# Performance work log

Hardware: AMD Instinct MI355X
Metric: run time of the kernel (lower is better)

Reference implementation:

```python
import jax, jax.numpy as jnp
import numpy as np

# Static dims (match init_kwargs / input_specs)
N, F, C, H, W = 1, 60, 31, 64, 64
DIM = 60          # embed dim == F
WS = 8            # window_size
NH = 6            # num_heads
HD = DIM // NH    # head dim = 10
SHIFT = WS // 2   # shift for odd blocks
NWIN_TOK = WS * WS
MLP_HID = 4 * DIM
EPS = 1e-5


def _rel_pos_index(ws):
    # standard Swin relative position index, computed once in numpy
    coords = np.stack(np.meshgrid(np.arange(ws), np.arange(ws), indexing='ij'))  # (2, ws, ws)
    coords = coords.reshape(2, -1)                                                # (2, ws*ws)
    rel = coords[:, :, None] - coords[:, None, :]                                 # (2, n, n)
    rel = rel.transpose(1, 2, 0)
    rel[..., 0] += ws - 1
    rel[..., 1] += ws - 1
    rel[..., 0] *= 2 * ws - 1
    return rel.sum(-1)                                                            # (n, n)

RPI = jnp.asarray(_rel_pos_index(WS))  # (64, 64) int


def _attn_mask(h, w, ws, shift):
    # mask for shifted-window attention: -100 where tokens come from different regions
    img = np.zeros((h, w))
    cnt = 0
    for hs in (slice(0, -ws), slice(-ws, -shift), slice(-shift, None)):
        for wsl in (slice(0, -ws), slice(-ws, -shift), slice(-shift, None)):
            img[hs, wsl] = cnt
            cnt += 1
    m = img.reshape(h // ws, ws, w // ws, ws).transpose(0, 2, 1, 3).reshape(-1, ws * ws)  # (nW, n)
    diff = m[:, None, :] - m[:, :, None]
    return jnp.asarray(np.where(diff != 0, -100.0, 0.0).astype(np.float32))               # (nW, n, n)

ATTN_MASK = _attn_mask(H, W, WS, SHIFT)


def _ln(x, g, b):
    mu = jnp.mean(x, axis=-1, keepdims=True)
    var = jnp.mean(jnp.square(x - mu), axis=-1, keepdims=True)
    return (x - mu) * jax.lax.rsqrt(var + EPS) * g + b


def _swin_block(x, shift, g1, b1, qkv_w, qkv_b, rpb, proj_w, proj_b,
                g2, b2, fc1_w, fc1_b, fc2_w, fc2_b):
    # x: (B, L=H*W, DIM)
    B = x.shape[0]
    shortcut = x
    h = _ln(x, g1, b1).reshape(B, H, W, DIM)
    if shift > 0:
        h = jnp.roll(h, (-shift, -shift), axis=(1, 2))
    # window partition -> (B*nW, n, DIM)
    win = h.reshape(B, H // WS, WS, W // WS, WS, DIM).transpose(0, 1, 3, 2, 4, 5)
    win = win.reshape(-1, NWIN_TOK, DIM)
    Bw = win.shape[0]
    # qkv projection (torch Linear: y = x @ W.T + b)
    qkv = win @ qkv_w.T + qkv_b                                   # (Bw, n, 3*DIM)
    qkv = qkv.reshape(Bw, NWIN_TOK, 3, NH, HD).transpose(2, 0, 3, 1, 4)
    q, k, v = qkv[0], qkv[1], qkv[2]                              # (Bw, NH, n, HD)
    scale = HD ** -0.5
    attn = jnp.einsum('bhnd,bhmd->bhnm', q * scale, k)            # (Bw, NH, n, n)
    bias = rpb[RPI.reshape(-1)].reshape(NWIN_TOK, NWIN_TOK, NH).transpose(2, 0, 1)
    attn = attn + bias[None]
    if shift > 0:
        nW = ATTN_MASK.shape[0]
        attn = attn.reshape(-1, nW, NH, NWIN_TOK, NWIN_TOK) + ATTN_MASK[None, :, None]
        attn = attn.reshape(-1, NH, NWIN_TOK, NWIN_TOK)
    attn = jax.nn.softmax(attn, axis=-1)
    out = jnp.einsum('bhnm,bhmd->bhnd', attn, v).transpose(0, 2, 1, 3).reshape(Bw, NWIN_TOK, DIM)
    out = out @ proj_w.T + proj_b
    # window reverse -> (B, H, W, DIM)
    out = out.reshape(B, H // WS, W // WS, WS, WS, DIM).transpose(0, 1, 3, 2, 4, 5)
    out = out.reshape(B, H, W, DIM)
    if shift > 0:
        out = jnp.roll(out, (shift, shift), axis=(1, 2))
    x = shortcut + out.reshape(B, H * W, DIM)
    # MLP with exact GELU (torch nn.GELU default)
    h2 = _ln(x, g2, b2)
    h2 = jax.nn.gelu(h2 @ fc1_w.T + fc1_b, approximate=False) @ fc2_w.T + fc2_b
    return x + h2


def setup_inputs() -> dict:
    key = jax.random.key(0)
    ks = jax.random.split(key, 16)
    s = 0.02
    inp = {
        'x': jax.random.normal(ks[0], (N, F, C, H, W), jnp.float32),
        'norm1_g': jnp.ones((2, DIM), jnp.float32),
        'norm1_b': jnp.zeros((2, DIM), jnp.float32),
        'qkv_w': jax.random.normal(ks[1], (2, 3 * DIM, DIM), jnp.float32) * s,
        'qkv_b': jnp.zeros((2, 3 * DIM), jnp.float32),
        'rpb': jax.random.normal(ks[2], (2, (2 * WS - 1) ** 2, NH), jnp.float32) * s,
        'proj_w': jax.random.normal(ks[3], (2, DIM, DIM), jnp.float32) * s,
        'proj_b': jnp.zeros((2, DIM), jnp.float32),
        'norm2_g': jnp.ones((2, DIM), jnp.float32),
        'norm2_b': jnp.zeros((2, DIM), jnp.float32),
        'fc1_w': jax.random.normal(ks[4], (2, MLP_HID, DIM), jnp.float32) * s,
        'fc1_b': jnp.zeros((2, MLP_HID), jnp.float32),
        'fc2_w': jax.random.normal(ks[5], (2, DIM, MLP_HID), jnp.float32) * s,
        'fc2_b': jnp.zeros((2, DIM), jnp.float32),
    }
    return inp


def reference(x, norm1_g, norm1_b, qkv_w, qkv_b, rpb, proj_w, proj_b,
              norm2_g, norm2_b, fc1_w, fc1_b, fc2_w, fc2_b):
    # (N, F, C, H, W) -> (N*C, F, H, W) -> patch embed (flatten) -> (B, L, DIM)
    out = jnp.transpose(x, (0, 2, 1, 3, 4)).reshape(N * C, F, H, W)
    out = out.reshape(N * C, F, H * W).transpose(0, 2, 1)  # (B, L, DIM)
    for i in range(2):
        shift = 0 if i % 2 == 0 else SHIFT
        out = _swin_block(out, shift,
                          norm1_g[i], norm1_b[i], qkv_w[i], qkv_b[i], rpb[i],
                          proj_w[i], proj_b[i], norm2_g[i], norm2_b[i],
                          fc1_w[i], fc1_b[i], fc2_w[i], fc2_b[i])
    # patch unembed -> (B, F, H, W) -> (N, C, F, H, W) -> transpose(1,2)
    out = out.transpose(0, 2, 1).reshape(N * C, F, H, W)
    out = out.reshape(N, C, F, H, W)
    return jnp.transpose(out, (0, 2, 1, 3, 4))
```

## Files before the change

kernel.cpp:

```cpp
#include <hip/hip_runtime.h>
#include <hip/hip_bf16.h>
#include <math.h>


#define NB 31
#define NTOK 4096
#define DIM 60
#define NTOT (NB*NTOK)
#define QK_SCALE 0.31622776601683794f

typedef __attribute__((ext_vector_type(8))) short bf16x8;
typedef __attribute__((ext_vector_type(4))) float f32x4;

__device__ __forceinline__ short f2b(float f){
    return __builtin_bit_cast(short, __float2bfloat16(f));
}
__device__ __forceinline__ float b2f(unsigned short u){
    union{unsigned u;float f;}v; v.u=((unsigned)u)<<16; return v.f;
}
__device__ __forceinline__ unsigned pk2(float a,float b){
    return (unsigned)(unsigned short)f2b(a) | ((unsigned)(unsigned short)f2b(b)<<16);
}
#define MFMA16(a,b,c) __builtin_amdgcn_mfma_f32_16x16x32_bf16(a,b,c,0,0,0)

#define PK_QKV  0
#define PK_PROJ 13824
#define PK_W1   18432
#define PK_W2   35712
#define PK_STRIDE 52608

__global__ __launch_bounds__(256) void pack_w(
    const float* __restrict__ qkv_w, const float* __restrict__ proj_w,
    const float* __restrict__ fc1_w, const float* __restrict__ fc2_w,
    const float* __restrict__ rpb, short* __restrict__ pk, float* __restrict__ btab)
{
    const int L = blockIdx.x;
    short* o = pk + (size_t)L * PK_STRIDE;
    const float* qw = qkv_w + L * 10800;
    const float* pw = proj_w + L * 3600;
    const float* w1 = fc1_w + L * 14400;
    const float* w2 = fc2_w + L * 14400;
    const float* rp = rpb + L * 1350;
    const int t0 = blockIdx.y * 256 + threadIdx.x;
    const int STP = 256 * 8;

    for (int i = t0; i < 192 * 72; i += STP) {
        int row = i / 72, k = i - row * 72;
        int p = row / 96, rg = row - p * 96;
        short v = 0;
        if (rg < 90 && k < 60) {
            int which = rg / 30, idx = rg - which * 30;
            int h = p * 3 + idx / 10, e = idx - (idx / 10) * 10;
            float wv = qw[(which * 60 + h * 10 + e) * 60 + k];
            if (which == 0) wv *= QK_SCALE;
            v = f2b(wv);
        }
        o[PK_QKV + i] = v;
    }
    for (int i = t0; i < 64 * 72; i += STP) {
        int n = i / 72, k = i - n * 72;
        o[PK_PROJ + i] = (n < 60 && k < 60) ? f2b(pw[n * 60 + k]) : (short)0;
    }
    for (int i = t0; i < 240 * 72; i += STP) {
        int n = i / 72, k = i - n * 72;
        o[PK_W1 + i] = (k < 60) ? f2b(w1[n * 60 + k]) : (short)0;
    }
    for (int i = t0; i < 64 * 264; i += STP) {
        int n = i / 264, k = i - n * 264;
        o[PK_W2 + i] = (n < 60 && k < 240) ? f2b(w2[n * 240 + k]) : (short)0;
    }
    float* bo = btab + (size_t)L * 4 * 24576;
    for (int i = t0; i < 4 * 24576; i += STP) {
        int c = i / 24576, rem = i - c * 24576;
        int h = rem >> 12, rem2 = rem & 4095;
        int ii = rem2 >> 6, j = rem2 & 63;
        int iy = ii >> 3, ix = ii & 7, jy = j >> 3, jx = j & 7;
        float v = rp[((iy - jy + 7) * 15 + (ix - jx + 7)) * 6 + h];
        int riy = (c & 2) ? (iy < 4 ? 1 : 2) : 0;
        int rix = (c & 1) ? (ix < 4 ? 1 : 2) : 0;
        int rjy = (c & 2) ? (jy < 4 ? 1 : 2) : 0;
        int rjx = (c & 1) ? (jx < 4 ? 1 : 2) : 0;
        if (riy != rjy || rix != rjx) v -= 100.f;
        bo[i] = v;
    }
}

template<int L>
__global__ __launch_bounds__(256, 5) void swin_layer(
    const void* __restrict__ xin_v, void* __restrict__ xout_v,
    const float* __restrict__ g1, const float* __restrict__ b1,
    const float* __restrict__ g2, const float* __restrict__ b2,
    const short* __restrict__ pk, const float* __restrict__ btab,
    const float* __restrict__ qkv_b, const float* __restrict__ proj_b,
    const float* __restrict__ fc1_b, const float* __restrict__ fc2_b)
{
    __shared__ __attribute__((aligned(16))) short R1[64 * 72];
    __shared__ __attribute__((aligned(16))) short R2[10112];

    const f32x4 Z4 = {0.f, 0.f, 0.f, 0.f};
    const bf16x8 Z8 = {0, 0, 0, 0, 0, 0, 0, 0};

    const int tid = threadIdx.x, blk = blockIdx.x;
    const int b = blk >> 6, w = blk & 63, wy = w >> 3, wx = w & 7;
    const int shift = L ? 4 : 0;
    const int cls = L ? (((wy == 7) ? 2 : 0) + ((wx == 7) ? 1 : 0)) : 0;

    const float* xf = (const float*)xin_v;
    const unsigned short* xb = (const unsigned short*)xin_v;

    for (int i = tid; i < 64 * 18; i += 256) {
        int row = i / 18, t = i - row * 18, bc = t / 3, k = t - bc * 3;
        *(int*)&R2[row * 104 + bc * 16 + 10 + 2 * k] = 0;
    }
    for (int i = tid; i < 3 * 216; i += 256) {
        int hl = i / 216, j = i - hl * 216;
        *(int*)&R2[6656 + (hl * 16 + 10) * 72 + 2 * j] = 0;
    }

    const int tk = tid >> 2, l4 = tid & 3;
    const int tok = (((wy * 8 + (tk >> 3) + shift) & 63) << 6)
                  + ((wx * 8 + (tk & 7) + shift) & 63);
    if (L == 0) {
        float xr[15]; float s = 0.f, s2 = 0.f;
#pragma unroll
        for (int dd = 0; dd < 15; ++dd) {
            float v = xf[(size_t)(l4 * 15 + dd) * NTOT + b * NTOK + tok];
            xr[dd] = v; s += v; s2 += v * v;
        }
        s  += __shfl_xor(s, 1);  s  += __shfl_xor(s, 2);
        s2 += __shfl_xor(s2, 1); s2 += __shfl_xor(s2, 2);
        const float mu = s * (1.f / 60.f);
        const float rs = rsqrtf(s2 * (1.f / 60.f) - mu * mu + 1e-5f);
#pragma unroll
        for (int dd = 0; dd < 15; ++dd) {
            int d = l4 * 15 + dd;
            R1[tk * 72 + d] = f2b((xr[dd] - mu) * rs * g1[d] + b1[d]);
        }
#pragma unroll
        for (int u = 0; u < 3; ++u) R1[tk * 72 + 60 + l4 * 3 + u] = 0;
    } else {
        float xr[16]; float s = 0.f, s2 = 0.f;
        const int nd = (l4 == 3) ? 6 : 8, c0 = l4 * 16;
        const unsigned* rp_ = (const unsigned*)(xb + ((size_t)b * NTOK + tok) * DIM) + l4 * 8;
#pragma unroll
        for (int j = 0; j < 8; ++j) {
            if (j < nd) {
                unsigned u = rp_[j];
                float v0 = b2f((unsigned short)(u & 0xffff));
                float v1 = b2f((unsigned short)(u >> 16));
                xr[2 * j] = v0; xr[2 * j + 1] = v1;
                s += v0 + v1; s2 += v0 * v0 + v1 * v1;
            }
        }
        s  += __shfl_xor(s, 1);  s  += __shfl_xor(s, 2);
        s2 += __shfl_xor(s2, 1); s2 += __shfl_xor(s2, 2);
        const float mu = s * (1.f / 60.f);
        const float rs = rsqrtf(s2 * (1.f / 60.f) - mu * mu + 1e-5f);
#pragma unroll
        for (int j = 0; j < 8; ++j) {
            if (j < nd) {
                int d = c0 + 2 * j;
                float n0 = (xr[2 * j] - mu) * rs * g1[d] + b1[d];
                float n1 = (xr[2 * j + 1] - mu) * rs * g1[d + 1] + b1[d + 1];
                *(unsigned*)&R1[tk * 72 + d] = pk2(n0, n1);
            }
        }
        if (l4 == 3) {
#pragma unroll
            for (int u = 0; u < 3; ++u) *(unsigned*)&R1[tk * 72 + 60 + 2 * u] = 0;
        }
    }

    const int lane = tid & 63, r16 = lane & 15, g = lane >> 4;
    const int m0 = (tid >> 6) << 4;

    int tok4[4];
#pragma unroll
    for (int r = 0; r < 4; ++r) {
        int row = m0 + g * 4 + r;
        tok4[r] = (((wy * 8 + (row >> 3) + shift) & 63) << 6)
                + ((wx * 8 + (row & 7) + shift) & 63);
    }

    bf16x8 a0 = *(const bf16x8*)&R1[(m0 + r16) * 72 + g * 8];
    bf16x8 a1 = *(const bf16x8*)&R1[(m0 + r16) * 72 + 32 + g * 8];
    const float* btc = btab + (size_t)cls * 24576 + (m0 + r16) * 64;

    for (int p = 0; p < 2; ++p) {
#pragma unroll
        for (int nt = 0; nt < 6; ++nt) {
            const short* wr = pk + PK_QKV + (size_t)(p * 96 + nt * 16 + r16) * 72;
            bf16x8 w0 = *(const bf16x8*)(wr + g * 8);
            bf16x8 w1v = *(const bf16x8*)(wr + 32 + g * 8);
            int c = nt * 16 + r16;
            int which = 0, hl = 0, e = 0; float bias = 0.f;
            if (c < 90) {
                which = c / 30; int idx = c - which * 30;
                hl = idx / 10; e = idx - hl * 10;
                bias = qkv_b[which * 60 + (p * 3 + hl) * 10 + e];
                if (which == 0) bias *= QK_SCALE;
            }
            f32x4 acc = {bias, bias, bias, bias};
            acc = MFMA16(a0, w0, acc);
            acc = MFMA16(a1, w1v, acc);
            if (c < 90) {
                if (which == 0) {
#pragma unroll
                    for (int r = 0; r < 4; ++r)
                        R2[(m0 + g * 4 + r) * 104 + hl * 16 + e] = f2b(acc[r]);
                } else if (which == 1) {
#pragma unroll
                    for (int r = 0; r < 4; ++r)
                        R2[(m0 + g * 4 + r) * 104 + 48 + hl * 16 + e] = f2b(acc[r]);
                } else {
#pragma unroll
                    for (int r = 0; r < 2; ++r)
                        *(unsigned*)&R2[6656 + (hl * 16 + e) * 72 + m0 + g * 4 + 2 * r] =
                            pk2(acc[2 * r], acc[2 * r + 1]);
                }
            }
        }
        __syncthreads();

        for (int hl = 0; hl < 3; ++hl) {
            const int h = p * 3 + hl;
            bf16x8 qa = Z8;
            if (g < 2) qa = *(const bf16x8*)&R2[(m0 + r16) * 104 + hl * 16 + g * 8];
            const float* bh = btc + h * 4096;
            f32x4 sv[4];
#pragma unroll
            for (int nt = 0; nt < 4; ++nt) {
                bf16x8 kb = Z8;
                if (g < 2) kb = *(const bf16x8*)&R2[(nt * 16 + r16) * 104 + 48 + hl * 16 + g * 8];
                sv[nt] = MFMA16(kb, qa, *(const f32x4*)&bh[nt * 16 + g * 4]);
            }
            float mx = -1e30f;
#pragma unroll
            for (int nt = 0; nt < 4; ++nt)
#pragma unroll
                for (int r = 0; r < 4; ++r) mx = fmaxf(mx, sv[nt][r]);
            mx = fmaxf(mx, __shfl_xor(mx, 16));
            mx = fmaxf(mx, __shfl_xor(mx, 32));
            float sum = 0.f;
#pragma unroll
            for (int nt = 0; nt < 4; ++nt)
#pragma unroll
                for (int r = 0; r < 4; ++r) {
                    float e = __expf(sv[nt][r] - mx);
                    sv[nt][r] = e; sum += e;
                }
            sum += __shfl_xor(sum, 16);
            sum += __shfl_xor(sum, 32);
            const float inv = 1.f / sum;

            unsigned qd00 = pk2(sv[0][0], sv[0][1]), qd01 = pk2(sv[0][2], sv[0][3]);
            unsigned qd10 = pk2(sv[1][0], sv[1][1]), qd11 = pk2(sv[1][2], sv[1][3]);
            unsigned qd20 = pk2(sv[2][0], sv[2][1]), qd21 = pk2(sv[2][2], sv[2][3]);
            unsigned qd30 = pk2(sv[3][0], sv[3][1]), qd31 = pk2(sv[3][2], sv[3][3]);
            const int sA = (r16 + ((g & 1) << 5)) << 2;
            const int sB = sA + 64;
            const bool hi = (g >> 1) & 1;
            union { unsigned u[4]; bf16x8 v; } pb0, pb1;
            {
                unsigned x0 = __builtin_amdgcn_ds_bpermute(sA, (int)qd00);
                unsigned y0 = __builtin_amdgcn_ds_bpermute(sA, (int)qd10);
                pb0.u[0] = hi ? y0 : x0;
                unsigned x1 = __builtin_amdgcn_ds_bpermute(sA, (int)qd01);
                unsigned y1 = __builtin_amdgcn_ds_bpermute(sA, (int)qd11);
                pb0.u[1] = hi ? y1 : x1;
                unsigned x2 = __builtin_amdgcn_ds_bpermute(sB, (int)qd00);
                unsigned y2 = __builtin_amdgcn_ds_bpermute(sB, (int)qd10);
                pb0.u[2] = hi ? y2 : x2;
                unsigned x3 = __builtin_amdgcn_ds_bpermute(sB, (int)qd01);
                unsigned y3 = __builtin_amdgcn_ds_bpermute(sB, (int)qd11);
                pb0.u[3] = hi ? y3 : x3;
                unsigned u0 = __builtin_amdgcn_ds_bpermute(sA, (int)qd20);
                unsigned v0 = __builtin_amdgcn_ds_bpermute(sA, (int)qd30);
                pb1.u[0] = hi ? v0 : u0;
                unsigned u1 = __builtin_amdgcn_ds_bpermute(sA, (int)qd21);
                unsigned v1 = __builtin_amdgcn_ds_bpermute(sA, (int)qd31);
                pb1.u[1] = hi ? v1 : u1;
                unsigned u2 = __builtin_amdgcn_ds_bpermute(sB, (int)qd20);
                unsigned v2 = __builtin_amdgcn_ds_bpermute(sB, (int)qd30);
                pb1.u[2] = hi ? v2 : u2;
                unsigned u3 = __builtin_amdgcn_ds_bpermute(sB, (int)qd21);
                unsigned v3 = __builtin_amdgcn_ds_bpermute(sB, (int)qd31);
                pb1.u[3] = hi ? v3 : u3;
            }
            bf16x8 va0 = *(const bf16x8*)&R2[6656 + (hl * 16 + r16) * 72 + g * 8];
            bf16x8 va1 = *(const bf16x8*)&R2[6656 + (hl * 16 + r16) * 72 + 32 + g * 8];
            f32x4 o = MFMA16(va0, pb0.v, Z4);
            o = MFMA16(va1, pb1.v, o);
            if (g < 2) {
                *(unsigned*)&R1[(m0 + r16) * 72 + h * 10 + g * 4]     = pk2(o[0] * inv, o[1] * inv);
                *(unsigned*)&R1[(m0 + r16) * 72 + h * 10 + g * 4 + 2] = pk2(o[2] * inv, o[3] * inv);
            } else if (g == 2) {
                *(unsigned*)&R1[(m0 + r16) * 72 + h * 10 + 8] = pk2(o[0] * inv, o[1] * inv);
            }
        }
        __syncthreads();
    }

    {
        bf16x8 oa0 = *(const bf16x8*)&R1[(m0 + r16) * 72 + g * 8];
        bf16x8 oa1 = *(const bf16x8*)&R1[(m0 + r16) * 72 + 32 + g * 8];
#pragma unroll
        for (int nt = 0; nt < 4; ++nt) {
            const short* wr = pk + PK_PROJ + (size_t)(nt * 16 + r16) * 72;
            bf16x8 w0 = *(const bf16x8*)(wr + g * 8);
            bf16x8 w1v = *(const bf16x8*)(wr + 32 + g * 8);
            int d = nt * 16 + r16;
            float pb_ = (d < 60) ? proj_b[d] : 0.f;
            f32x4 acc = {pb_, pb_, pb_, pb_};
            acc = MFMA16(oa0, w0, acc);
            acc = MFMA16(oa1, w1v, acc);
            if (d < 60) {
#pragma unroll
                for (int r = 0; r < 4; ++r) {
                    float res;
                    if (L == 0) res = xf[(size_t)d * NTOT + b * NTOK + tok4[r]];
                    else        res = b2f(xb[((size_t)b * NTOK + tok4[r]) * DIM + d]);
                    R1[(m0 + g * 4 + r) * 72 + d] = f2b(res + acc[r]);
                }
            }
        }
    }

    {
        float yr[15]; float s = 0.f, s2 = 0.f;
#pragma unroll
        for (int dd = 0; dd < 15; ++dd) {
            float v = b2f((unsigned short)R1[tk * 72 + dd * 4 + l4]);
            yr[dd] = v; s += v; s2 += v * v;
        }
        s  += __shfl_xor(s, 1);  s  += __shfl_xor(s, 2);
        s2 += __shfl_xor(s2, 1); s2 += __shfl_xor(s2, 2);
        const float mu = s * (1.f / 60.f);
        const float rs = rsqrtf(s2 * (1.f / 60.f) - mu * mu + 1e-5f);
#pragma unroll
        for (int dd = 0; dd < 15; ++dd) {
            int d = dd * 4 + l4;
            R2[tk * 136 + d] = f2b((yr[dd] - mu) * rs * g2[d] + b2[d]);
        }
#pragma unroll
        for (int u = 0; u < 3; ++u) R2[tk * 136 + 60 + l4 * 3 + u] = 0;
    }

    bf16x8 la0 = *(const bf16x8*)&R2[(m0 + r16) * 136 + g * 8];
    bf16x8 la1 = *(const bf16x8*)&R2[(m0 + r16) * 136 + 32 + g * 8];

    f32x4 acc2[4];
#pragma unroll
    for (int nt = 0; nt < 4; ++nt) {
        int d = nt * 16 + r16;
        float fb = (d < 60) ? fc2_b[d] : 0.f;
        acc2[nt] = (f32x4){fb, fb, fb, fb};
    }

#pragma unroll
    for (int nt = 0; nt < 8; ++nt) {
        const short* wr = pk + PK_W1 + (size_t)(nt * 16 + r16) * 72;
        bf16x8 w0 = *(const bf16x8*)(wr + g * 8);
        bf16x8 w1v = *(const bf16x8*)(wr + 32 + g * 8);
        int c = nt * 16 + r16;
        float fb = fc1_b[c];
        f32x4 acc = {fb, fb, fb, fb};
        acc = MFMA16(la0, w0, acc);
        acc = MFMA16(la1, w1v, acc);
#pragma unroll
        for (int r = 0; r < 4; ++r) {
            float u = acc[r];
            float zz = 1.5957691216057308f * u + 0.07135481178528657f * (u * u * u);
            float ge = u * __builtin_amdgcn_rcpf(1.f + __expf(-zz));
            R2[(m0 + g * 4 + r) * 136 + c] = f2b(ge);
        }
    }
#pragma unroll
    for (int kk = 0; kk < 4; ++kk) {
        bf16x8 ha = *(const bf16x8*)&R2[(m0 + r16) * 136 + kk * 32 + g * 8];
#pragma unroll
        for (int nt = 0; nt < 4; ++nt) {
            const short* wr = pk + PK_W2 + (size_t)(nt * 16 + r16) * 264 + kk * 32 + g * 8;
            acc2[nt] = MFMA16(ha, *(const bf16x8*)wr, acc2[nt]);
        }
    }
    *(int*)&R2[(m0 + r16) * 136 + 112 + g * 4]     = 0;
    *(int*)&R2[(m0 + r16) * 136 + 112 + g * 4 + 2] = 0;
#pragma unroll
    for (int nt = 0; nt < 7; ++nt) {
        const short* wr = pk + PK_W1 + (size_t)(128 + nt * 16 + r16) * 72;
        bf16x8 w0 = *(const bf16x8*)(wr + g * 8);
        bf16x8 w1v = *(const bf16x8*)(wr + 32 + g * 8);
        int c = nt * 16 + r16;
        float fb = fc1_b[128 + c];
        f32x4 acc = {fb, fb, fb, fb};
        acc = MFMA16(la0, w0, acc);
        acc = MFMA16(la1, w1v, acc);
#pragma unroll
        for (int r = 0; r < 4; ++r) {
            float u = acc[r];
            float zz = 1.5957691216057308f * u + 0.07135481178528657f * (u * u * u);
            float ge = u * __builtin_amdgcn_rcpf(1.f + __expf(-zz));
            R2[(m0 + g * 4 + r) * 136 + c] = f2b(ge);
        }
    }
#pragma unroll
    for (int kk = 0; kk < 4; ++kk) {
        bf16x8 ha = *(const bf16x8*)&R2[(m0 + r16) * 136 + kk * 32 + g * 8];
#pragma unroll
        for (int nt = 0; nt < 4; ++nt) {
            const short* wr = pk + PK_W2 + (size_t)(nt * 16 + r16) * 264 + 128 + kk * 32 + g * 8;
            acc2[nt] = MFMA16(ha, *(const bf16x8*)wr, acc2[nt]);
        }
    }

#pragma unroll
    for (int nt = 0; nt < 4; ++nt) {
        int d = nt * 16 + r16;
        if (d < 60) {
#pragma unroll
            for (int r = 0; r < 4; ++r) {
                float yv = b2f((unsigned short)R1[(m0 + g * 4 + r) * 72 + d]);
                float v = yv + acc2[nt][r];
                if (L == 0) R2[(m0 + g * 4 + r) * 136 + d] = f2b(v);
                else        ((float*)R2)[(m0 + g * 4 + r) * 68 + d] = v;
            }
        }
    }
    __syncthreads();

    if (L == 0) {
        unsigned* ob = (unsigned*)xout_v;
        const size_t gbase = (size_t)b * NTOK * 30;
        for (int i = tid; i < 1920; i += 256) {
            int r = i / 30, c = i - r * 30;
            int gt = ((wy * 8 + (r >> 3)) << 6) + wx * 8 + (r & 7);
            ob[gbase + (size_t)gt * 30 + c] = *(unsigned*)&R2[r * 136 + 2 * c];
        }
    } else {
        float* of = (float*)xout_v;
        for (int i = tid; i < 3840; i += 256) {
            int d = i >> 6, t = i & 63;
            int gt = (((wy * 8 + (t >> 3) + 4) & 63) << 6) + ((wx * 8 + (t & 7) + 4) & 63);
            of[(size_t)d * NTOT + b * NTOK + gt] = ((const float*)R2)[t * 68 + d];
        }
    }
}

extern "C" void kernel_launch(void* const* d_in, const int* in_sizes, int n_in,
                              void* d_out, int out_size, void* d_ws, size_t ws_size,
                              hipStream_t stream)
{
    const float* x       = (const float*)d_in[0];
    const float* norm1_g = (const float*)d_in[1];
    const float* norm1_b = (const float*)d_in[2];
    const float* qkv_w   = (const float*)d_in[3];
    const float* qkv_b   = (const float*)d_in[4];
    const float* rpb     = (const float*)d_in[5];
    const float* proj_w  = (const float*)d_in[6];
    const float* proj_b  = (const float*)d_in[7];
    const float* norm2_g = (const float*)d_in[8];
    const float* norm2_b = (const float*)d_in[9];
    const float* fc1_w   = (const float*)d_in[10];
    const float* fc1_b   = (const float*)d_in[11];
    const float* fc2_w   = (const float*)d_in[12];
    const float* fc2_b   = (const float*)d_in[13];

    unsigned short* bufA = (unsigned short*)d_ws;
    short* pk  = (short*)((char*)d_ws + (size_t)NTOT * DIM * 2);
    float* btab = (float*)((char*)pk + 2 * PK_STRIDE * 2);

    dim3 block(256);
    pack_w<<<dim3(2, 8), block, 0, stream>>>(qkv_w, proj_w, fc1_w, fc2_w, rpb, pk, btab);

    dim3 grid(NB * 64);
    swin_layer<0><<<grid, block, 0, stream>>>(
        (const void*)x, (void*)bufA,
        norm1_g, norm1_b, norm2_g, norm2_b, pk, btab,
        qkv_b, proj_b, fc1_b, fc2_b);
    swin_layer<1><<<grid, block, 0, stream>>>(
        (const void*)bufA, d_out,
        norm1_g + 60, norm1_b + 60, norm2_g + 60, norm2_b + 60,
        pk + PK_STRIDE, btab + 4 * 24576,
        qkv_b + 180, proj_b + 60, fc1_b + 240, fc2_b + 60);

    (void)in_sizes; (void)n_in; (void)out_size; (void)ws_size;
}
```

Before: 178.2 us.

## Keep input residual in registers and remap block index across XCDs

After: 176.4 us. No clear change (-1.0%).

```diff
diff --git a/kernel.cpp b/kernel.cpp
--- a/kernel.cpp
+++ b/kernel.cpp
@@ -100,7 +100,8 @@
     const f32x4 Z4 = {0.f, 0.f, 0.f, 0.f};
     const bf16x8 Z8 = {0, 0, 0, 0, 0, 0, 0, 0};
 
-    const int tid = threadIdx.x, blk = blockIdx.x;
+    const int tid = threadIdx.x;
+    const int blk = ((blockIdx.x & 7) * 248) + (blockIdx.x >> 3);
     const int b = blk >> 6, w = blk & 63, wy = w >> 3, wx = w & 7;
     const int shift = L ? 4 : 0;
     const int cls = L ? (((wy == 7) ? 2 : 0) + ((wx == 7) ? 1 : 0)) : 0;
@@ -120,6 +121,7 @@
     const int tk = tid >> 2, l4 = tid & 3;
     const int tok = (((wy * 8 + (tk >> 3) + shift) & 63) << 6)
                   + ((wx * 8 + (tk & 7) + shift) & 63);
+    unsigned xpk[8];
     if (L == 0) {
         float xr[15]; float s = 0.f, s2 = 0.f;
 #pragma unroll
@@ -138,6 +140,9 @@
         }
 #pragma unroll
         for (int u = 0; u < 3; ++u) R1[tk * 72 + 60 + l4 * 3 + u] = 0;
+#pragma unroll
+        for (int u = 0; u < 7; ++u) xpk[u] = pk2(xr[2 * u], xr[2 * u + 1]);
+        xpk[7] = pk2(xr[14], 0.f);
     } else {
         float xr[16]; float s = 0.f, s2 = 0.f;
         const int nd = (l4 == 3) ? 6 : 8, c0 = l4 * 16;
@@ -146,6 +151,7 @@
         for (int j = 0; j < 8; ++j) {
             if (j < nd) {
                 unsigned u = rp_[j];
+                xpk[j] = u;
                 float v0 = b2f((unsigned short)(u & 0xffff));
                 float v1 = b2f((unsigned short)(u >> 16));
                 xr[2 * j] = v0; xr[2 * j + 1] = v1;
@@ -173,14 +179,6 @@
 
     const int lane = tid & 63, r16 = lane & 15, g = lane >> 4;
     const int m0 = (tid >> 6) << 4;
-
-    int tok4[4];
-#pragma unroll
-    for (int r = 0; r < 4; ++r) {
-        int row = m0 + g * 4 + r;
-        tok4[r] = (((wy * 8 + (row >> 3) + shift) & 63) << 6)
-                + ((wx * 8 + (row & 7) + shift) & 63);
-    }
 
     bf16x8 a0 = *(const bf16x8*)&R1[(m0 + r16) * 72 + g * 8];
     bf16x8 a1 = *(const bf16x8*)&R1[(m0 + r16) * 72 + 32 + g * 8];
@@ -316,22 +314,21 @@
             acc = MFMA16(oa1, w1v, acc);
             if (d < 60) {
 #pragma unroll
-                for (int r = 0; r < 4; ++r) {
-                    float res;
-                    if (L == 0) res = xf[(size_t)d * NTOT + b * NTOK + tok4[r]];
-                    else        res = b2f(xb[((size_t)b * NTOK + tok4[r]) * DIM + d]);
-                    R1[(m0 + g * 4 + r) * 72 + d] = f2b(res + acc[r]);
-                }
-            }
-        }
-    }
-
-    {
-        float yr[15]; float s = 0.f, s2 = 0.f;
+                for (int r = 0; r < 4; ++r)
+                    R1[(m0 + g * 4 + r) * 72 + d] = f2b(acc[r]);
+            }
+        }
+    }
+
+    if (L == 0) {
+        float yv[15]; float s = 0.f, s2 = 0.f;
 #pragma unroll
         for (int dd = 0; dd < 15; ++dd) {
-            float v = b2f((unsigned short)R1[tk * 72 + dd * 4 + l4]);
-            yr[dd] = v; s += v; s2 += v * v;
+            int d = l4 * 15 + dd;
+            float xv = b2f((unsigned short)((dd & 1) ? (xpk[dd >> 1] >> 16)
+                                                    : (xpk[dd >> 1] & 0xffff)));
+            float y = xv + b2f((unsigned short)R1[tk * 72 + d]);
+            yv[dd] = y; s += y; s2 += y * y;
         }
         s  += __shfl_xor(s, 1);  s  += __shfl_xor(s, 2);
         s2 += __shfl_xor(s2, 1); s2 += __shfl_xor(s2, 2);
@@ -339,11 +336,45 @@
         const float rs = rsqrtf(s2 * (1.f / 60.f) - mu * mu + 1e-5f);
 #pragma unroll
         for (int dd = 0; dd < 15; ++dd) {
-            int d = dd * 4 + l4;
-            R2[tk * 136 + d] = f2b((yr[dd] - mu) * rs * g2[d] + b2[d]);
+            int d = l4 * 15 + dd;
+            R1[tk * 72 + d] = f2b(yv[dd]);
+            R2[tk * 136 + d] = f2b((yv[dd] - mu) * rs * g2[d] + b2[d]);
         }
 #pragma unroll
         for (int u = 0; u < 3; ++u) R2[tk * 136 + 60 + l4 * 3 + u] = 0;
+    } else {
+        float yv[16]; float s = 0.f, s2 = 0.f;
+        const int nd = (l4 == 3) ? 6 : 8, c0 = l4 * 16;
+#pragma unroll
+        for (int j = 0; j < 8; ++j) {
+            if (j < nd) {
+                int d = c0 + 2 * j;
+                float y0 = b2f((unsigned short)(xpk[j] & 0xffff))
+                         + b2f((unsigned short)R1[tk * 72 + d]);
+                float y1 = b2f((unsigned short)(xpk[j] >> 16))
+                         + b2f((unsigned short)R1[tk * 72 + d + 1]);
+                yv[2 * j] = y0; yv[2 * j + 1] = y1;
+                s += y0 + y1; s2 += y0 * y0 + y1 * y1;
+            }
+        }
+        s  += __shfl_xor(s, 1);  s  += __shfl_xor(s, 2);
+        s2 += __shfl_xor(s2, 1); s2 += __shfl_xor(s2, 2);
+        const float mu = s * (1.f / 60.f);
+        const float rs = rsqrtf(s2 * (1.f / 60.f) - mu * mu + 1e-5f);
+#pragma unroll
+        for (int j = 0; j < 8; ++j) {
+            if (j < nd) {
+                int d = c0 + 2 * j;
+                *(unsigned*)&R1[tk * 72 + d] = pk2(yv[2 * j], yv[2 * j + 1]);
+                float n0 = (yv[2 * j] - mu) * rs * g2[d] + b2[d];
+                float n1 = (yv[2 * j + 1] - mu) * rs * g2[d + 1] + b2[d + 1];
+                *(unsigned*)&R2[tk * 136 + d] = pk2(n0, n1);
+            }
+        }
+        if (l4 == 3) {
+#pragma unroll
+            for (int u = 0; u < 3; ++u) *(unsigned*)&R2[tk * 136 + 60 + 2 * u] = 0;
+        }
     }
 
     bf16x8 la0 = *(const bf16x8*)&R2[(m0 + r16) * 136 + g * 8];
```
